# Optimization experiments

Measured on AMD Instinct MI355X. Metric: run time of the kernel, lower is better.

Reference implementation:

```python
import jax, jax.numpy as jnp
import numpy as np

N, E, D, H = 50000, 500000, 128, 4
C = D // H
EPS = 1e-5


def _layer_norm(x, g, b):
    mu = jnp.mean(x, axis=-1, keepdims=True)
    var = jnp.mean((x - mu) ** 2, axis=-1, keepdims=True)
    return (x - mu) * jax.lax.rsqrt(var + EPS) * g + b


def setup_inputs() -> dict:
    key = jax.random.key(0)
    ks = jax.random.split(key, 20)
    f = lambda i, shape: jax.random.normal(ks[i], shape, dtype=jnp.float32) * 0.05
    return {
        "x": f(0, (N, D)),
        "edge_index": jax.random.randint(ks[1], (2, E), 0, N),
        "w_gcn": f(2, (D, D)), "b_gcn": f(3, (D,)),
        "wq": f(4, (D, D)), "bq": f(5, (D,)),
        "wk": f(6, (D, D)), "bk": f(7, (D,)),
        "wv": f(8, (D, D)), "bv": f(9, (D,)),
        "w_skip": f(10, (D, D)), "b_skip": f(11, (D,)),
        "w_beta": f(12, (3 * D, 1)),
        "g1": jnp.ones((D,), jnp.float32), "b1": jnp.zeros((D,), jnp.float32),
        "g2": jnp.ones((D,), jnp.float32), "b2": jnp.zeros((D,), jnp.float32),
        "w_rel": f(13, (D, 2 * D)), "w_root": f(14, (2 * D, D)),
        "local_w": jnp.ones((1,), jnp.float32), "global_w": jnp.ones((1,), jnp.float32),
    }


def reference(x, edge_index, w_gcn, b_gcn, wq, bq, wk, bk, wv, bv,
              w_skip, b_skip, w_beta, g1, b1, g2, b2, w_rel, w_root,
              local_w, global_w):
    src, dst = edge_index[0], edge_index[1]

    # ---- GCNConv (add_self_loops=False, symmetric norm) ----
    xw = x @ w_gcn                                   # [N, D]
    deg = jax.ops.segment_sum(jnp.ones((E,), x.dtype), dst, num_segments=N)
    dinv = jnp.where(deg > 0, jax.lax.rsqrt(jnp.maximum(deg, 1.0)), 0.0)
    coef = dinv[src] * dinv[dst]                     # [E]
    local_out = jax.ops.segment_sum(coef[:, None] * xw[src], dst, num_segments=N) + b_gcn

    # ---- TransformerConv (heads=4, concat=True, beta=True) ----
    q = (x @ wq + bq).reshape(N, H, C)
    k = (x @ wk + bk).reshape(N, H, C)
    v = (x @ wv + bv).reshape(N, H, C)
    alpha = jnp.sum(q[dst] * k[src], axis=-1) / jnp.sqrt(jnp.float32(C))  # [E, H]
    m = jax.ops.segment_max(alpha, dst, num_segments=N)
    m = jnp.where(jnp.isfinite(m), m, 0.0)
    a = jnp.exp(alpha - m[dst])
    s = jax.ops.segment_sum(a, dst, num_segments=N)
    attn = a / jnp.maximum(s[dst], 1e-16)            # [E, H] segment softmax over in-edges
    agg = jax.ops.segment_sum(attn[..., None] * v[src], dst, num_segments=N)
    out_g = agg.reshape(N, D)
    x_r = x @ w_skip + b_skip
    beta = jax.nn.sigmoid(jnp.concatenate([out_g, x_r, out_g - x_r], axis=-1) @ w_beta)
    global_out = beta * x_r + (1.0 - beta) * out_g

    # ---- combine + norm + FFN ----
    h = local_w * local_out + global_w * global_out
    h = _layer_norm(h + h, g1, b1)
    out = jax.nn.relu(h @ w_rel) @ w_root
    out = _layer_norm(out + h, g2, b2)
    return out
```

## Files before the change

### kernel.cpp

```cpp
#include <hip/hip_runtime.h>
#include <math.h>

#define D 128
#define EPSV 1e-5f

typedef unsigned short ushort_t;
typedef unsigned char uchar_t;
typedef __attribute__((ext_vector_type(8))) short short8v;
typedef __attribute__((ext_vector_type(4))) float f32x4;
typedef __attribute__((ext_vector_type(2))) float f32x2;
typedef _Float16 half_t;
typedef __attribute__((ext_vector_type(2))) _Float16 h2;

#if __has_builtin(__builtin_amdgcn_cvt_pk_f16_fp8)
#define HAVE_F16P 1
#else
#define HAVE_F16P 0
#endif

__device__ __forceinline__ float bf2f(unsigned u) {
    return __uint_as_float(u << 16);
}
__device__ __forceinline__ ushort_t f2bf(float f) {
    unsigned u = __float_as_uint(f);
    unsigned r = (u + 0x7fffu + ((u >> 16) & 1u)) >> 16;
    return (ushort_t)r;
}
__device__ __forceinline__ float bfp(uint4 v, int i) {
    unsigned w = (&v.x)[i >> 1];
    return bf2f((i & 1) ? (w >> 16) : (w & 0xffffu));
}

__device__ __forceinline__ ushort_t qconv(float f) {
#if HAVE_F16P
    half_t h = (half_t)f;
    return __builtin_bit_cast(ushort_t, h);
#else
    return f2bf(f);
#endif
}

#define UNPACK8_FP8(ux, uy, o) { \
    f32x2 _a = __builtin_amdgcn_cvt_pk_f32_fp8((int)(ux), false); \
    f32x2 _b = __builtin_amdgcn_cvt_pk_f32_fp8((int)(ux), true);  \
    f32x2 _c = __builtin_amdgcn_cvt_pk_f32_fp8((int)(uy), false); \
    f32x2 _d = __builtin_amdgcn_cvt_pk_f32_fp8((int)(uy), true);  \
    o[0] = _a.x; o[1] = _a.y; o[2] = _b.x; o[3] = _b.y;           \
    o[4] = _c.x; o[5] = _c.y; o[6] = _d.x; o[7] = _d.y; }

__device__ __forceinline__ unsigned bf4_to_fp8x4(unsigned w0, unsigned w1) {
    int u = __builtin_amdgcn_cvt_pk_fp8_f32(bf2f(w0 & 0xffffu), bf2f(w0 >> 16), 0, false);
    u = __builtin_amdgcn_cvt_pk_fp8_f32(bf2f(w1 & 0xffffu), bf2f(w1 >> 16), u, true);
    return (unsigned)u;
}

__device__ __forceinline__ h2 h2_shfl_xor_add(h2 a, int off) {
    return a + __builtin_bit_cast(h2, __shfl_xor(__builtin_bit_cast(int, a), off));
}

__global__ void cvt_deg_kernel(const float* __restrict__ in, ushort_t* __restrict__ out, int n8,
                               const int* __restrict__ dst, int* __restrict__ deg, int E)
{
    int i = blockIdx.x * blockDim.x + threadIdx.x;
    if (i < n8) {
        float4 a = reinterpret_cast<const float4*>(in)[i * 2];
        float4 b = reinterpret_cast<const float4*>(in)[i * 2 + 1];
        uint4 o;
        o.x = (unsigned)f2bf(a.x) | ((unsigned)f2bf(a.y) << 16);
        o.y = (unsigned)f2bf(a.z) | ((unsigned)f2bf(a.w) << 16);
        o.z = (unsigned)f2bf(b.x) | ((unsigned)f2bf(b.y) << 16);
        o.w = (unsigned)f2bf(b.z) | ((unsigned)f2bf(b.w) << 16);
        reinterpret_cast<uint4*>(out)[i] = o;
    }
    if (i < E) atomicAdd(&deg[dst[i]], 1);
}

__global__ __launch_bounds__(256)
void proj_gemm(const ushort_t* __restrict__ xbf,
               const ushort_t* __restrict__ Bt,
               const float* __restrict__ bias,
               const float* __restrict__ dinv,
               uchar_t* __restrict__ pack, ushort_t* __restrict__ qb,
               ushort_t* __restrict__ xrb, int M)
{
    __shared__ ushort_t Cs[128 * 136];
    const int tid = threadIdx.x, lane = tid & 63, wid = tid >> 6;
    const int wr = wid >> 1, wc = wid & 1;
    const int R0 = blockIdx.x * 128;
    const int ct = blockIdx.y;

    short8v av[4][4];
    #pragma unroll
    for (int r = 0; r < 4; ++r) {
        int gr = R0 + wr * 64 + r * 16 + (lane & 15);
        if (gr >= M) gr = M - 1;
        #pragma unroll
        for (int ks = 0; ks < 4; ++ks)
            av[r][ks] = *reinterpret_cast<const short8v*>(
                &xbf[(size_t)gr * 128 + ks * 32 + (lane >> 4) * 8]);
    }

    f32x4 acc[4][4] = {};
    #pragma unroll
    for (int ks = 0; ks < 4; ++ks) {
        short8v bv[4];
        #pragma unroll
        for (int c = 0; c < 4; ++c) {
            int col = ct * 128 + wc * 64 + c * 16 + (lane & 15);
            bv[c] = *reinterpret_cast<const short8v*>(
                &Bt[(size_t)col * 128 + ks * 32 + (lane >> 4) * 8]);
        }
        #pragma unroll
        for (int r = 0; r < 4; ++r)
            #pragma unroll
            for (int c = 0; c < 4; ++c)
                acc[r][c] = __builtin_amdgcn_mfma_f32_16x16x32_bf16(av[r][ks], bv[c], acc[r][c], 0, 0, 0);
    }

    #pragma unroll
    for (int r = 0; r < 4; ++r) {
        int rowb = wr * 64 + r * 16 + (lane >> 4) * 4;
        #pragma unroll
        for (int i = 0; i < 4; ++i) {
            float sc = 1.f;
            if (ct == 0) {
                int grow = R0 + rowb + i;
                if (grow >= M) grow = M - 1;
                sc = dinv[grow];
            }
            #pragma unroll
            for (int c = 0; c < 4; ++c) {
                int col = wc * 64 + c * 16 + (lane & 15);
                float val = acc[r][c][i] + bias[ct * 128 + col];
                if (ct == 0) val *= sc;
                Cs[(rowb + i) * 136 + col] = (ct == 1) ? qconv(val) : f2bf(val);
            }
        }
    }
    __syncthreads();

    if (ct == 1 || ct == 4) {
        #pragma unroll
        for (int it = 0; it < 8; ++it) {
            int linear = tid + it * 256;
            int row = linear >> 4, ch = linear & 15;
            int gr = R0 + row;
            if (gr < M) {
                uint4 v = *reinterpret_cast<const uint4*>(&Cs[row * 136 + ch * 8]);
                ushort_t* dst = (ct == 1) ? (qb + (size_t)gr * 128)
                                          : (xrb + (size_t)gr * 128);
                *reinterpret_cast<uint4*>(dst + ch * 8) = v;
            }
        }
    } else {
        #pragma unroll
        for (int it = 0; it < 4; ++it) {
            int linear = tid + it * 256;
            int row = linear >> 3, ch = linear & 7;
            int gr = R0 + row;
            if (gr < M) {
                uint4 lo = *reinterpret_cast<const uint4*>(&Cs[row * 136 + ch * 16]);
                uint4 hi = *reinterpret_cast<const uint4*>(&Cs[row * 136 + ch * 16 + 8]);
                uint4 o;
                o.x = bf4_to_fp8x4(lo.x, lo.y);
                o.y = bf4_to_fp8x4(lo.z, lo.w);
                o.z = bf4_to_fp8x4(hi.x, hi.y);
                o.w = bf4_to_fp8x4(hi.z, hi.w);
                uchar_t* prow = pack + (size_t)gr * 384;
                if (ct == 0) {
                    *reinterpret_cast<uint4*>(prow + 256 + ch * 16) = o;
                } else if (ct == 2) {
                    *reinterpret_cast<uint2*>(prow + (2 * ch) * 16)     = make_uint2(o.x, o.y);
                    *reinterpret_cast<uint2*>(prow + (2 * ch + 1) * 16) = make_uint2(o.z, o.w);
                } else {
                    *reinterpret_cast<uint2*>(prow + (2 * ch) * 16 + 8)     = make_uint2(o.x, o.y);
                    *reinterpret_cast<uint2*>(prow + (2 * ch + 1) * 16 + 8) = make_uint2(o.z, o.w);
                }
            }
        }
    }
}

__device__ __forceinline__ int swz(int ch, int row) {
    return (ch & 24) | ((ch ^ row) & 7);
}

__global__ __launch_bounds__(256)
void ffn_fused(const ushort_t* __restrict__ hlnb,
               const ushort_t* __restrict__ wt_rel,
               const ushort_t* __restrict__ wt_root,
               const float* __restrict__ g2, const float* __restrict__ b2,
               float* __restrict__ outf, int M)
{
    __shared__ float smem[128 * 130];
    ushort_t* Hs = (ushort_t*)smem;
    const int tid = threadIdx.x, lane = tid & 63, wid = tid >> 6;
    const int wr = wid >> 1, wc = wid & 1;
    const int R0 = blockIdx.x * 128;

    short8v av[4][4];
    #pragma unroll
    for (int r = 0; r < 4; ++r) {
        int gr = R0 + wr * 64 + r * 16 + (lane & 15);
        if (gr >= M) gr = M - 1;
        #pragma unroll
        for (int ks = 0; ks < 4; ++ks)
            av[r][ks] = *reinterpret_cast<const short8v*>(
                &hlnb[(size_t)gr * 128 + ks * 32 + (lane >> 4) * 8]);
    }
    for (int ct = 0; ct < 2; ++ct) {
        f32x4 acc[4][4] = {};
        #pragma unroll
        for (int ks = 0; ks < 4; ++ks) {
            short8v bv[4];
            #pragma unroll
            for (int c = 0; c < 4; ++c) {
                int col = ct * 128 + wc * 64 + c * 16 + (lane & 15);
                bv[c] = *reinterpret_cast<const short8v*>(
                    &wt_rel[(size_t)col * 128 + ks * 32 + (lane >> 4) * 8]);
            }
            #pragma unroll
            for (int r = 0; r < 4; ++r)
                #pragma unroll
                for (int c = 0; c < 4; ++c)
                    acc[r][c] = __builtin_amdgcn_mfma_f32_16x16x32_bf16(av[r][ks], bv[c], acc[r][c], 0, 0, 0);
        }
        #pragma unroll
        for (int r = 0; r < 4; ++r) {
            int rowb = wr * 64 + r * 16 + (lane >> 4) * 4;
            #pragma unroll
            for (int i = 0; i < 4; ++i)
                #pragma unroll
                for (int c = 0; c < 4; ++c) {
                    int row = rowb + i;
                    int col = ct * 128 + wc * 64 + c * 16 + (lane & 15);
                    int ch = col >> 3, el = col & 7;
                    Hs[row * 256 + swz(ch, row) * 8 + el] = f2bf(fmaxf(acc[r][c][i], 0.f));
                }
        }
    }
    __syncthreads();

    f32x4 acc2[4][4] = {};
    #pragma unroll
    for (int ks = 0; ks < 8; ++ks) {
        short8v a2[4], bv[4];
        #pragma unroll
        for (int r = 0; r < 4; ++r) {
            int row = wr * 64 + r * 16 + (lane & 15);
            int ch = ks * 4 + (lane >> 4);
            a2[r] = *reinterpret_cast<const short8v*>(&Hs[row * 256 + swz(ch, row) * 8]);
        }
        #pragma unroll
        for (int c = 0; c < 4; ++c) {
            int col = wc * 64 + c * 16 + (lane & 15);
            bv[c] = *reinterpret_cast<const short8v*>(
                &wt_root[(size_t)col * 256 + ks * 32 + (lane >> 4) * 8]);
        }
        #pragma unroll
        for (int r = 0; r < 4; ++r)
            #pragma unroll
            for (int c = 0; c < 4; ++c)
                acc2[r][c] = __builtin_amdgcn_mfma_f32_16x16x32_bf16(a2[r], bv[c], acc2[r][c], 0, 0, 0);
    }
    __syncthreads();

    float* Cs = smem;
    #pragma unroll
    for (int r = 0; r < 4; ++r) {
        int rowb = wr * 64 + r * 16 + (lane >> 4) * 4;
        #pragma unroll
        for (int i = 0; i < 4; ++i)
            #pragma unroll
            for (int c = 0; c < 4; ++c)
                Cs[(rowb + i) * 130 + wc * 64 + c * 16 + (lane & 15)] = acc2[r][c][i];
    }
    __syncthreads();

    const float ga = g2[lane * 2], gb = g2[lane * 2 + 1];
    const float ba = b2[lane * 2], bb2 = b2[lane * 2 + 1];
    for (int rr = 0; rr < 32; ++rr) {
        int row = wid * 32 + rr;
        int gr = R0 + row;
        if (gr >= M) break;
        unsigned hu = *reinterpret_cast<const unsigned*>(&hlnb[(size_t)gr * 128 + lane * 2]);
        float t0 = Cs[row * 130 + lane * 2]     + bf2f(hu & 0xffffu);
        float t1 = Cs[row * 130 + lane * 2 + 1] + bf2f(hu >> 16);
        float ssum = t0 + t1;
        #pragma unroll
        for (int off = 1; off <= 32; off <<= 1) ssum += __shfl_xor(ssum, off);
        float mu = ssum * (1.f / 128.f);
        float dv0 = t0 - mu, dv1 = t1 - mu;
        float vsum = dv0 * dv0 + dv1 * dv1;
        #pragma unroll
        for (int off = 1; off <= 32; off <<= 1) vsum += __shfl_xor(vsum, off);
        float rs = rsqrtf(vsum * (1.f / 128.f) + EPSV);
        float2 o = make_float2(dv0 * rs * ga + ba, dv1 * rs * gb + bb2);
        *reinterpret_cast<float2*>(&outf[(size_t)gr * 128 + lane * 2]) = o;
    }
}

__global__ __launch_bounds__(256)
void scan1_packw_kernel(const int* __restrict__ deg, int* __restrict__ row_start,
                        int* __restrict__ bsum, int n, int SB,
                        const float* __restrict__ wg, const float* __restrict__ wq,
                        const float* __restrict__ wk, const float* __restrict__ wv,
                        const float* __restrict__ wsk,
                        const float* __restrict__ bq, const float* __restrict__ bk,
                        const float* __restrict__ bv, const float* __restrict__ bsk,
                        const float* __restrict__ wrel, const float* __restrict__ wroot,
                        ushort_t* __restrict__ wt_all, ushort_t* __restrict__ wt_rel,
                        ushort_t* __restrict__ wt_root, float* __restrict__ bias_all)
{
    __shared__ int ws[4];
    if ((int)blockIdx.x < SB) {
        const int t = threadIdx.x, lane = t & 63, wid = t >> 6;
        const int base = blockIdx.x * 1024 + t * 4;
        int v0 = 0, v1 = 0, v2 = 0, v3 = 0;
        if (base + 3 < n) {
            int4 q = *reinterpret_cast<const int4*>(&deg[base]);
            v0 = q.x; v1 = q.y; v2 = q.z; v3 = q.w;
        } else {
            if (base < n)     v0 = deg[base];
            if (base + 1 < n) v1 = deg[base + 1];
            if (base + 2 < n) v2 = deg[base + 2];
            if (base + 3 < n) v3 = deg[base + 3];
        }
        int tot = v0 + v1 + v2 + v3;
        int inc = tot;
        #pragma unroll
        for (int off = 1; off < 64; off <<= 1) {
            int y = __shfl_up(inc, off);
            if (lane >= off) inc += y;
        }
        if (lane == 63) ws[wid] = inc;
        __syncthreads();
        int woff = 0;
        for (int w = 0; w < wid; ++w) woff += ws[w];
        int excl = woff + inc - tot;
        if (base < n)     row_start[base]     = excl;
        if (base + 1 < n) row_start[base + 1] = excl + v0;
        if (base + 2 < n) row_start[base + 2] = excl + v0 + v1;
        if (base + 3 < n) row_start[base + 3] = excl + v0 + v1 + v2;
        if (t == 0) bsum[blockIdx.x] = ws[0] + ws[1] + ws[2] + ws[3];
    } else {
        int i = (blockIdx.x - SB) * 256 + threadIdx.x;
        if (i < 640 * 128) {
            int c = i >> 7, k = i & 127;
            const float* srcs[5] = {wg, wq, wk, wv, wsk};
            wt_all[i] = f2bf(srcs[c >> 7][k * 128 + (c & 127)]);
        } else if (i < 640 * 128 + 256 * 128) {
            int j = i - 640 * 128;
            int c = j >> 7, k = j & 127;
            wt_rel[j] = f2bf(wrel[k * 256 + c]);
        } else if (i < 640 * 128 + 256 * 128 + 128 * 256) {
            int j = i - (640 * 128 + 256 * 128);
            int c = j >> 8, k = j & 255;
            wt_root[j] = f2bf(wroot[k * 128 + c]);
        } else if (i < 640 * 128 + 256 * 128 + 128 * 256 + 640) {
            int c = i - (640 * 128 + 256 * 128 + 128 * 256);
            float b = 0.f;
            if (c >= 128) {
                const float* bs[4] = {bq, bk, bv, bsk};
                b = bs[(c - 128) >> 7][c & 127];
            }
            bias_all[c] = b;
        }
    }
}

__global__ __launch_bounds__(256)
void scan3_kernel(const int* __restrict__ deg, const int* __restrict__ bsum,
                  int* __restrict__ row_start, int* __restrict__ cursor,
                  float* __restrict__ dinv, int n, int E)
{
    __shared__ int boff_s;
    const int K = blockIdx.x >> 2;
    const int t = threadIdx.x;
    if (t < 64) {
        int v = 0;
        for (int j = t; j < K; j += 64) v += bsum[j];
        #pragma unroll
        for (int off = 1; off <= 32; off <<= 1) v += __shfl_xor(v, off);
        if (t == 0) boff_s = v;
    }
    __syncthreads();
    int i = blockIdx.x * 256 + t;
    if (i < n) {
        int rs = row_start[i] + boff_s;
        row_start[i] = rs;
        cursor[i] = rs;
        int d = deg[i];
        dinv[i] = (d > 0) ? rsqrtf((float)d) : 0.f;
    }
    if (i == 0) row_start[n] = E;
}

__global__ void fill_kernel(const int* __restrict__ src, const int* __restrict__ dst,
                            int* __restrict__ cursor, int* __restrict__ csr_src, int E)
{
    int e = (blockIdx.x * blockDim.x + threadIdx.x) * 2;
    if (e + 1 < E) {
        int2 s2 = *reinterpret_cast<const int2*>(&src[e]);
        int2 d2 = *reinterpret_cast<const int2*>(&dst[e]);
        int p0 = atomicAdd(&cursor[d2.x], 1);
        csr_src[p0] = s2.x;
        int p1 = atomicAdd(&cursor[d2.y], 1);
        csr_src[p1] = s2.y;
    } else if (e < E) {
        int d = dst[e];
        int pos = atomicAdd(&cursor[d], 1);
        csr_src[pos] = src[e];
    }
}

__global__ __launch_bounds__(256)
void edge_fused_kernel(const uchar_t* __restrict__ pack,
                       const ushort_t* __restrict__ qbf,
                       const ushort_t* __restrict__ xrbf,
                       const int* __restrict__ row_start,
                       const int* __restrict__ csr_src,
                       const float* __restrict__ dinv,
                       const float* __restrict__ b_gcn,
                       const float* __restrict__ w_beta,
                       const float* __restrict__ g1, const float* __restrict__ b1,
                       const float* __restrict__ local_w, const float* __restrict__ global_w,
                       ushort_t* __restrict__ hln_bf, int n)
{
    const int wid = threadIdx.x >> 6, lane = threadIdx.x & 63;
    const int node = blockIdx.x * 4 + wid;
    if (node >= n) return;
    const int slot = lane >> 4, li = lane & 15;
    const int d8 = li * 8;

    const int e0 = row_start[node], e1 = row_start[node + 1];
    const int cnt = e1 - e0;
    const float dn = dinv[node];
    const float scale = 0.17677669529663687f;

    float s = 0.f;
    float va[8], ga[8];

#if HAVE_F16P
    uint4 qu = *reinterpret_cast<const uint4*>(&qbf[(size_t)node * 128 + d8]);
    h2 qh[4] = { __builtin_bit_cast(h2, qu.x), __builtin_bit_cast(h2, qu.y),
                 __builtin_bit_cast(h2, qu.z), __builtin_bit_cast(h2, qu.w) };
    h2 va2[4] = {}, ga2[4] = {};
    for (int j = e0; j < e1; j += 4) {
        const int je = j + slot;
        const int sidx = (je < e1) ? csr_src[je] : n;
        const uchar_t* prow = pack + (size_t)sidx * 384;
        uint4 kv = *reinterpret_cast<const uint4*>(prow + li * 16);
        uint2 xu = *reinterpret_cast<const uint2*>(prow + 256 + li * 8);
        h2 k0 = __builtin_amdgcn_cvt_pk_f16_fp8((short)(kv.x & 0xffffu));
        h2 k1 = __builtin_amdgcn_cvt_pk_f16_fp8((short)(kv.x >> 16));
        h2 k2 = __builtin_amdgcn_cvt_pk_f16_fp8((short)(kv.y & 0xffffu));
        h2 k3 = __builtin_amdgcn_cvt_pk_f16_fp8((short)(kv.y >> 16));
        float p = __builtin_amdgcn_fdot2(k0, qh[0], 0.f, false);
        p = __builtin_amdgcn_fdot2(k1, qh[1], p, false);
        p = __builtin_amdgcn_fdot2(k2, qh[2], p, false);
        p = __builtin_amdgcn_fdot2(k3, qh[3], p, false);
        p += __shfl_xor(p, 1);
        p += __shfl_xor(p, 2);
        float wgt = __expf(p * scale);
        s += wgt;
        half_t wh = (half_t)wgt;
        h2 w2 = { wh, wh };
        h2 v0 = __builtin_amdgcn_cvt_pk_f16_fp8((short)(kv.z & 0xffffu));
        h2 v1 = __builtin_amdgcn_cvt_pk_f16_fp8((short)(kv.z >> 16));
        h2 v2 = __builtin_amdgcn_cvt_pk_f16_fp8((short)(kv.w & 0xffffu));
        h2 v3 = __builtin_amdgcn_cvt_pk_f16_fp8((short)(kv.w >> 16));
        va2[0] += w2 * v0; va2[1] += w2 * v1; va2[2] += w2 * v2; va2[3] += w2 * v3;
        h2 x0 = __builtin_amdgcn_cvt_pk_f16_fp8((short)(xu.x & 0xffffu));
        h2 x1 = __builtin_amdgcn_cvt_pk_f16_fp8((short)(xu.x >> 16));
        h2 x2 = __builtin_amdgcn_cvt_pk_f16_fp8((short)(xu.y & 0xffffu));
        h2 x3 = __builtin_amdgcn_cvt_pk_f16_fp8((short)(xu.y >> 16));
        ga2[0] += x0; ga2[1] += x1; ga2[2] += x2; ga2[3] += x3;
    }
    #pragma unroll
    for (int off = 16; off <= 32; off <<= 1) {
        #pragma unroll
        for (int i = 0; i < 4; ++i) {
            va2[i] = h2_shfl_xor_add(va2[i], off);
            ga2[i] = h2_shfl_xor_add(ga2[i], off);
        }
    }
    #pragma unroll
    for (int i = 0; i < 4; ++i) {
        va[2 * i] = (float)va2[i][0]; va[2 * i + 1] = (float)va2[i][1];
        ga[2 * i] = (float)ga2[i][0]; ga[2 * i + 1] = (float)ga2[i][1];
    }
#else
    uint4 qu = *reinterpret_cast<const uint4*>(&qbf[(size_t)node * 128 + d8]);
    float q[8];
    #pragma unroll
    for (int i = 0; i < 8; ++i) q[i] = bfp(qu, i);
    #pragma unroll
    for (int i = 0; i < 8; ++i) { va[i] = 0.f; ga[i] = 0.f; }
    for (int j = e0; j < e1; j += 4) {
        const int je = j + slot;
        const int sidx = (je < e1) ? csr_src[je] : n;
        const uchar_t* prow = pack + (size_t)sidx * 384;
        uint4 kv = *reinterpret_cast<const uint4*>(prow + li * 16);
        uint2 xu = *reinterpret_cast<const uint2*>(prow + 256 + li * 8);
        float kf[8], vf[8], xf[8];
        UNPACK8_FP8(kv.x, kv.y, kf);
        UNPACK8_FP8(kv.z, kv.w, vf);
        UNPACK8_FP8(xu.x, xu.y, xf);
        float p = 0.f;
        #pragma unroll
        for (int i = 0; i < 8; ++i) p = fmaf(q[i], kf[i], p);
        p += __shfl_xor(p, 1);
        p += __shfl_xor(p, 2);
        float wgt = __expf(p * scale);
        s += wgt;
        #pragma unroll
        for (int i = 0; i < 8; ++i) {
            va[i] = fmaf(wgt, vf[i], va[i]);
            ga[i] += xf[i];
        }
    }
    #pragma unroll
    for (int off = 16; off <= 32; off <<= 1) {
        #pragma unroll
        for (int i = 0; i < 8; ++i) {
            va[i] += __shfl_xor(va[i], off);
            ga[i] += __shfl_xor(ga[i], off);
        }
    }
#endif

    s += __shfl_xor(s, 16);
    s += __shfl_xor(s, 32);
    if (cnt > 0) s -= (float)((4 - (cnt & 3)) & 3);
    const float denom = fmaxf(s, 1e-16f);

    uint4 xru = *reinterpret_cast<const uint4*>(&xrbf[(size_t)node * 128 + d8]);
    float t[8];
    float part = 0.f;
    #pragma unroll
    for (int i = 0; i < 8; ++i) {
        float og = va[i] / denom;
        float xr = bfp(xru, i);
        float lo = dn * ga[i] + b_gcn[d8 + i];
        part += og * w_beta[d8 + i] + xr * w_beta[128 + d8 + i]
              + (og - xr) * w_beta[256 + d8 + i];
        t[i] = lo;
        va[i] = og; ga[i] = xr;
    }
    #pragma unroll
    for (int off = 1; off <= 8; off <<= 1) part += __shfl_xor(part, off);
    const float beta = 1.f / (1.f + __expf(-part));

    const float lw = local_w[0], gw = global_w[0];
    float ssum = 0.f;
    #pragma unroll
    for (int i = 0; i < 8; ++i) {
        float go = beta * ga[i] + (1.f - beta) * va[i];
        t[i] = 2.f * (lw * t[i] + gw * go);
        ssum += t[i];
    }
    #pragma unroll
    for (int off = 1; off <= 8; off <<= 1) ssum += __shfl_xor(ssum, off);
    const float mu = ssum * (1.f / 128.f);
    float vsum = 0.f;
    #pragma unroll
    for (int i = 0; i < 8; ++i) { float d = t[i] - mu; vsum += d * d; }
    #pragma unroll
    for (int off = 1; off <= 8; off <<= 1) vsum += __shfl_xor(vsum, off);
    const float rs = rsqrtf(vsum * (1.f / 128.f) + EPSV);

    if (slot == 0) {
        uint4 o;
        #pragma unroll
        for (int i = 0; i < 4; ++i) {
            float o0 = (t[2*i]   - mu) * rs * g1[d8 + 2*i]   + b1[d8 + 2*i];
            float o1 = (t[2*i+1] - mu) * rs * g1[d8 + 2*i+1] + b1[d8 + 2*i+1];
            (&o.x)[i] = (unsigned)f2bf(o0) | ((unsigned)f2bf(o1) << 16);
        }
        *reinterpret_cast<uint4*>(&hln_bf[(size_t)node * 128 + d8]) = o;
    }
}

extern "C" void kernel_launch(void* const* d_in, const int* in_sizes, int n_in,
                              void* d_out, int out_size, void* d_ws, size_t ws_size,
                              hipStream_t stream)
{
    const float* x      = (const float*)d_in[0];
    const int*   ei     = (const int*)d_in[1];
    const float* w_gcn  = (const float*)d_in[2];
    const float* b_gcn  = (const float*)d_in[3];
    const float* wq     = (const float*)d_in[4];
    const float* bq     = (const float*)d_in[5];
    const float* wk     = (const float*)d_in[6];
    const float* bk     = (const float*)d_in[7];
    const float* wv     = (const float*)d_in[8];
    const float* bv     = (const float*)d_in[9];
    const float* w_skip = (const float*)d_in[10];
    const float* b_skip = (const float*)d_in[11];
    const float* w_beta = (const float*)d_in[12];
    const float* g1     = (const float*)d_in[13];
    const float* b1     = (const float*)d_in[14];
    const float* g2     = (const float*)d_in[15];
    const float* b2     = (const float*)d_in[16];
    const float* w_rel  = (const float*)d_in[17];
    const float* w_root = (const float*)d_in[18];
    const float* lw     = (const float*)d_in[19];
    const float* gw     = (const float*)d_in[20];

    const int N = in_sizes[0] / D;
    const int E = in_sizes[1] / 2;
    const int* src = ei;
    const int* dst = ei + E;

    char* wsb = (char*)d_ws;
    size_t off = 0;
    auto alloc = [&](size_t bytes) -> void* {
        void* p = wsb + off;
        off += (bytes + 255) & ~(size_t)255;
        return p;
    };
    uchar_t*  pack_kvx = (uchar_t*)alloc((size_t)(N + 1) * 384);
    ushort_t* xbf      = (ushort_t*)alloc((size_t)N * 128 * 2);
    ushort_t* qb_bf    = (ushort_t*)alloc((size_t)N * 128 * 2);
    ushort_t* xr_bf    = (ushort_t*)alloc((size_t)N * 128 * 2);
    ushort_t* hln_bf   = (ushort_t*)alloc((size_t)N * 128 * 2);
    ushort_t* wt_all   = (ushort_t*)alloc(640 * 128 * 2);
    ushort_t* wt_rel   = (ushort_t*)alloc(256 * 128 * 2);
    ushort_t* wt_root  = (ushort_t*)alloc(128 * 256 * 2);
    float*    bias_all = (float*)alloc(640 * 4);
    int*      deg      = (int*)alloc((size_t)N * 4);
    int*      row_start= (int*)alloc((size_t)(N + 1) * 4);
    int*      cursor   = (int*)alloc((size_t)N * 4);
    int*      csr_src  = (int*)alloc((size_t)E * 4);
    float*    dinv     = (float*)alloc((size_t)N * 4);
    int*      bsum     = (int*)alloc(((size_t)(N + 1023) / 1024) * 4);

    float* out = (float*)d_out;
    const int SB = (N + 1023) / 1024;
    const int n8 = N * 16;

    hipMemsetAsync(deg, 0, (size_t)N * sizeof(int), stream);
    hipMemsetAsync(pack_kvx + (size_t)N * 384, 0, 384, stream);
    {
        int work = (n8 > E) ? n8 : E;
        cvt_deg_kernel<<<dim3((work + 255) / 256), dim3(256), 0, stream>>>(
            x, xbf, n8, dst, deg, E);
    }
    scan1_packw_kernel<<<dim3(SB + 579), dim3(256), 0, stream>>>(
        deg, row_start, bsum, N, SB,
        w_gcn, wq, wk, wv, w_skip, bq, bk, bv, b_skip, w_rel, w_root,
        wt_all, wt_rel, wt_root, bias_all);
    scan3_kernel<<<dim3((N + 255) / 256), dim3(256), 0, stream>>>(
        deg, bsum, row_start, cursor, dinv, N, E);
    fill_kernel<<<dim3((E / 2 + 255) / 256), dim3(256), 0, stream>>>(src, dst, cursor, csr_src, E);

    const int MB = (N + 127) / 128;
    proj_gemm<<<dim3(MB, 5), dim3(256), 0, stream>>>(
        xbf, wt_all, bias_all, dinv, pack_kvx, qb_bf, xr_bf, N);

    edge_fused_kernel<<<dim3((N + 3) / 4), dim3(256), 0, stream>>>(
        pack_kvx, qb_bf, xr_bf, row_start, csr_src, dinv, b_gcn, w_beta,
        g1, b1, lw, gw, hln_bf, N);

    ffn_fused<<<dim3(MB), dim3(256), 0, stream>>>(
        hln_bf, wt_rel, wt_root, g2, b2, out, N);
}
```

Baseline: 206.3 us.

## Pad CSR rows to multiples of four and use a 512-byte packed row stride

Each node's CSR segment is padded to a multiple of four edges, and the padding slots point at a zero dummy row. This removes the per-edge bounds check in the edge loops. The packed K/V/X row stride goes from 384 to 512 bytes, so the address is a shift, at the cost of more memory and more gather bandwidth footprint. The softmax scale and log2(e) are folded into Q in the projection GEMM, so the edge loop can use exp2f directly. The extra padding writes run inside the fill kernel.

```diff
diff --git a/kernel.cpp b/kernel.cpp
--- a/kernel.cpp
+++ b/kernel.cpp
@@ -17,6 +17,8 @@
 #else
 #define HAVE_F16P 0
 #endif
+
+#define QKS (0.17677669529663687f * 1.4426950408889634f)
 
 __device__ __forceinline__ float bf2f(unsigned u) {
     return __uint_as_float(u << 16);
@@ -133,6 +135,7 @@
                 int col = wc * 64 + c * 16 + (lane & 15);
                 float val = acc[r][c][i] + bias[ct * 128 + col];
                 if (ct == 0) val *= sc;
+                if (ct == 1) val *= QKS;
                 Cs[(rowb + i) * 136 + col] = (ct == 1) ? qconv(val) : f2bf(val);
             }
         }
@@ -166,7 +169,7 @@
                 o.y = bf4_to_fp8x4(lo.z, lo.w);
                 o.z = bf4_to_fp8x4(hi.x, hi.y);
                 o.w = bf4_to_fp8x4(hi.z, hi.w);
-                uchar_t* prow = pack + (size_t)gr * 384;
+                uchar_t* prow = pack + ((size_t)gr << 9);
                 if (ct == 0) {
                     *reinterpret_cast<uint4*>(prow + 256 + ch * 16) = o;
                 } else if (ct == 2) {
@@ -326,7 +329,9 @@
             if (base + 2 < n) v2 = deg[base + 2];
             if (base + 3 < n) v3 = deg[base + 3];
         }
-        int tot = v0 + v1 + v2 + v3;
+        int p0 = (v0 + 3) & ~3, p1 = (v1 + 3) & ~3;
+        int p2 = (v2 + 3) & ~3, p3 = (v3 + 3) & ~3;
+        int tot = p0 + p1 + p2 + p3;
         int inc = tot;
         #pragma unroll
         for (int off = 1; off < 64; off <<= 1) {
@@ -339,9 +344,9 @@
         for (int w = 0; w < wid; ++w) woff += ws[w];
         int excl = woff + inc - tot;
         if (base < n)     row_start[base]     = excl;
-        if (base + 1 < n) row_start[base + 1] = excl + v0;
-        if (base + 2 < n) row_start[base + 2] = excl + v0 + v1;
-        if (base + 3 < n) row_start[base + 3] = excl + v0 + v1 + v2;
+        if (base + 1 < n) row_start[base + 1] = excl + p0;
+        if (base + 2 < n) row_start[base + 2] = excl + p0 + p1;
+        if (base + 3 < n) row_start[base + 3] = excl + p0 + p1 + p2;
         if (t == 0) bsum[blockIdx.x] = ws[0] + ws[1] + ws[2] + ws[3];
     } else {
         int i = (blockIdx.x - SB) * 256 + threadIdx.x;
@@ -372,7 +377,7 @@
 __global__ __launch_bounds__(256)
 void scan3_kernel(const int* __restrict__ deg, const int* __restrict__ bsum,
                   int* __restrict__ row_start, int* __restrict__ cursor,
-                  float* __restrict__ dinv, int n, int E)
+                  float* __restrict__ dinv, int n)
 {
     __shared__ int boff_s;
     const int K = blockIdx.x >> 2;
@@ -392,25 +397,37 @@
         cursor[i] = rs;
         int d = deg[i];
         dinv[i] = (d > 0) ? rsqrtf((float)d) : 0.f;
-    }
-    if (i == 0) row_start[n] = E;
+        if (i == n - 1) row_start[n] = rs + ((d + 3) & ~3);
+    }
 }
 
 __global__ void fill_kernel(const int* __restrict__ src, const int* __restrict__ dst,
-                            int* __restrict__ cursor, int* __restrict__ csr_src, int E)
-{
-    int e = (blockIdx.x * blockDim.x + threadIdx.x) * 2;
-    if (e + 1 < E) {
-        int2 s2 = *reinterpret_cast<const int2*>(&src[e]);
-        int2 d2 = *reinterpret_cast<const int2*>(&dst[e]);
-        int p0 = atomicAdd(&cursor[d2.x], 1);
-        csr_src[p0] = s2.x;
-        int p1 = atomicAdd(&cursor[d2.y], 1);
-        csr_src[p1] = s2.y;
-    } else if (e < E) {
-        int d = dst[e];
-        int pos = atomicAdd(&cursor[d], 1);
-        csr_src[pos] = src[e];
+                            int* __restrict__ cursor, int* __restrict__ csr_src,
+                            const int* __restrict__ row_start, const int* __restrict__ deg,
+                            int E, int EH, int n)
+{
+    int t = blockIdx.x * blockDim.x + threadIdx.x;
+    if (t < EH) {
+        int e = t * 2;
+        if (e + 1 < E) {
+            int2 s2 = *reinterpret_cast<const int2*>(&src[e]);
+            int2 d2 = *reinterpret_cast<const int2*>(&dst[e]);
+            int p0 = atomicAdd(&cursor[d2.x], 1);
+            csr_src[p0] = s2.x;
+            int p1 = atomicAdd(&cursor[d2.y], 1);
+            csr_src[p1] = s2.y;
+        } else if (e < E) {
+            int d = dst[e];
+            int pos = atomicAdd(&cursor[d], 1);
+            csr_src[pos] = src[e];
+        }
+    } else {
+        int i = t - EH;
+        if (i < n) {
+            int rs = row_start[i], d = deg[i];
+            int pd = (d + 3) & ~3;
+            for (int j = rs + d; j < rs + pd; ++j) csr_src[j] = n;
+        }
     }
 }
 
@@ -420,6 +437,7 @@
                        const ushort_t* __restrict__ xrbf,
                        const int* __restrict__ row_start,
                        const int* __restrict__ csr_src,
+                       const int* __restrict__ degp,
                        const float* __restrict__ dinv,
                        const float* __restrict__ b_gcn,
                        const float* __restrict__ w_beta,
@@ -434,9 +452,8 @@
     const int d8 = li * 8;
 
     const int e0 = row_start[node], e1 = row_start[node + 1];
-    const int cnt = e1 - e0;
+    const int cnt = degp[node];
     const float dn = dinv[node];
-    const float scale = 0.17677669529663687f;
 
     float s = 0.f;
     float va[8], ga[8];
@@ -447,9 +464,8 @@
                  __builtin_bit_cast(h2, qu.z), __builtin_bit_cast(h2, qu.w) };
     h2 va2[4] = {}, ga2[4] = {};
     for (int j = e0; j < e1; j += 4) {
-        const int je = j + slot;
-        const int sidx = (je < e1) ? csr_src[je] : n;
-        const uchar_t* prow = pack + (size_t)sidx * 384;
+        const int sidx = csr_src[j + slot];
+        const uchar_t* prow = pack + ((size_t)sidx << 9);
         uint4 kv = *reinterpret_cast<const uint4*>(prow + li * 16);
         uint2 xu = *reinterpret_cast<const uint2*>(prow + 256 + li * 8);
         h2 k0 = __builtin_amdgcn_cvt_pk_f16_fp8((short)(kv.x & 0xffffu));
@@ -462,7 +478,7 @@
         p = __builtin_amdgcn_fdot2(k3, qh[3], p, false);
         p += __shfl_xor(p, 1);
         p += __shfl_xor(p, 2);
-        float wgt = __expf(p * scale);
+        float wgt = exp2f(p);
         s += wgt;
         half_t wh = (half_t)wgt;
         h2 w2 = { wh, wh };
@@ -498,9 +514,8 @@
     #pragma unroll
     for (int i = 0; i < 8; ++i) { va[i] = 0.f; ga[i] = 0.f; }
     for (int j = e0; j < e1; j += 4) {
-        const int je = j + slot;
-        const int sidx = (je < e1) ? csr_src[je] : n;
-        const uchar_t* prow = pack + (size_t)sidx * 384;
+        const int sidx = csr_src[j + slot];
+        const uchar_t* prow = pack + ((size_t)sidx << 9);
         uint4 kv = *reinterpret_cast<const uint4*>(prow + li * 16);
         uint2 xu = *reinterpret_cast<const uint2*>(prow + 256 + li * 8);
         float kf[8], vf[8], xf[8];
@@ -512,7 +527,7 @@
         for (int i = 0; i < 8; ++i) p = fmaf(q[i], kf[i], p);
         p += __shfl_xor(p, 1);
         p += __shfl_xor(p, 2);
-        float wgt = __expf(p * scale);
+        float wgt = exp2f(p);
         s += wgt;
         #pragma unroll
         for (int i = 0; i < 8; ++i) {
@@ -532,7 +547,7 @@
 
     s += __shfl_xor(s, 16);
     s += __shfl_xor(s, 32);
-    if (cnt > 0) s -= (float)((4 - (cnt & 3)) & 3);
+    s -= (float)((e1 - e0) - cnt);
     const float denom = fmaxf(s, 1e-16f);
 
     uint4 xru = *reinterpret_cast<const uint4*>(&xrbf[(size_t)node * 128 + d8]);
@@ -620,7 +635,7 @@
         off += (bytes + 255) & ~(size_t)255;
         return p;
     };
-    uchar_t*  pack_kvx = (uchar_t*)alloc((size_t)(N + 1) * 384);
+    uchar_t*  pack_kvx = (uchar_t*)alloc((size_t)(N + 1) * 512);
     ushort_t* xbf      = (ushort_t*)alloc((size_t)N * 128 * 2);
     ushort_t* qb_bf    = (ushort_t*)alloc((size_t)N * 128 * 2);
     ushort_t* xr_bf    = (ushort_t*)alloc((size_t)N * 128 * 2);
@@ -632,16 +647,17 @@
     int*      deg      = (int*)alloc((size_t)N * 4);
     int*      row_start= (int*)alloc((size_t)(N + 1) * 4);
     int*      cursor   = (int*)alloc((size_t)N * 4);
-    int*      csr_src  = (int*)alloc((size_t)E * 4);
+    int*      csr_src  = (int*)alloc((size_t)(E + 3 * (size_t)N + 4) * 4);
     float*    dinv     = (float*)alloc((size_t)N * 4);
     int*      bsum     = (int*)alloc(((size_t)(N + 1023) / 1024) * 4);
 
     float* out = (float*)d_out;
     const int SB = (N + 1023) / 1024;
     const int n8 = N * 16;
+    const int EH = (E + 1) / 2;
 
     hipMemsetAsync(deg, 0, (size_t)N * sizeof(int), stream);
-    hipMemsetAsync(pack_kvx + (size_t)N * 384, 0, 384, stream);
+    hipMemsetAsync(pack_kvx + (size_t)N * 512, 0, 512, stream);
     {
         int work = (n8 > E) ? n8 : E;
         cvt_deg_kernel<<<dim3((work + 255) / 256), dim3(256), 0, stream>>>(
@@ -652,15 +668,16 @@
         w_gcn, wq, wk, wv, w_skip, bq, bk, bv, b_skip, w_rel, w_root,
         wt_all, wt_rel, wt_root, bias_all);
     scan3_kernel<<<dim3((N + 255) / 256), dim3(256), 0, stream>>>(
-        deg, bsum, row_start, cursor, dinv, N, E);
-    fill_kernel<<<dim3((E / 2 + 255) / 256), dim3(256), 0, stream>>>(src, dst, cursor, csr_src, E);
+        deg, bsum, row_start, cursor, dinv, N);
+    fill_kernel<<<dim3((EH + N + 255) / 256), dim3(256), 0, stream>>>(
+        src, dst, cursor, csr_src, row_start, deg, E, EH, N);
 
     const int MB = (N + 127) / 128;
     proj_gemm<<<dim3(MB, 5), dim3(256), 0, stream>>>(
         xbf, wt_all, bias_all, dinv, pack_kvx, qb_bf, xr_bf, N);
 
     edge_fused_kernel<<<dim3((N + 3) / 4), dim3(256), 0, stream>>>(
-        pack_kvx, qb_bf, xr_bf, row_start, csr_src, dinv, b_gcn, w_beta,
+        pack_kvx, qb_bf, xr_bf, row_start, csr_src, deg, dinv, b_gcn, w_beta,
         g1, b1, lw, gw, hln_bf, N);
 
     ffn_fused<<<dim3(MB), dim3(256), 0, stream>>>(
```

New measurement: 209.2 us. Within noise of the previous version (+1.4%).
